# Optimization experiments

Hardware: AMD Instinct MI355X
Metric: run time of the kernel (lower is better)

## Reference

```python
import jax, jax.numpy as jnp
import numpy as np

B, D_IN, D_HID, D_OUT = 32768, 512, 4096, 512
EPS = 1e-12  # F.normalize eps


def setup_inputs() -> dict:
    key = jax.random.key(0)
    ks = jax.random.split(key, 9)
    # Weights scaled up from the original 0.001 init so the norm_max clamp
    # branch is actually exercised (norms vary around the threshold).
    return {
        "x": jax.random.normal(ks[0], (B, D_IN), jnp.float32),
        "in_mean": jax.random.normal(ks[1], (D_IN,), jnp.float32) * 0.1,
        "in_std": jax.random.uniform(ks[2], (D_IN,), jnp.float32, 0.5, 1.5),
        "out_mean": jax.random.normal(ks[3], (D_OUT,), jnp.float32) * 0.1,
        "out_std": jax.random.uniform(ks[4], (D_OUT,), jnp.float32, 0.5, 1.5),
        "W1": jax.random.normal(ks[5], (D_HID, D_IN), jnp.float32) * 0.02,
        "b1": jax.random.normal(ks[6], (D_HID,), jnp.float32) * 0.001,
        "W2": jax.random.normal(ks[7], (D_OUT, D_HID), jnp.float32) * 0.02,
        "b2": jax.random.normal(ks[8], (D_OUT,), jnp.float32) * 0.001,
        "norm_max": 1,
    }


def reference(x, in_mean, in_std, out_mean, out_std, W1, b1, W2, b2, norm_max):
    norm_max = jnp.float32(norm_max)
    x_copy = x[..., :512]
    # input normalization
    xn = (x - in_mean) / in_std
    # 2-layer MLP: Linear -> ReLU -> Linear
    h = jax.nn.relu(jnp.einsum("bi,hi->bh", xn, W1) + b1)
    res = jnp.einsum("bh,oh->bo", h, W2) + b2
    # vectorized per-row norm clamp (torch loop: rescale rows with norm > norm_max)
    norms = jnp.linalg.norm(res, axis=-1, keepdims=True)  # [B,1]
    scale = norm_max / jax.lax.stop_gradient(norms)
    res = jnp.where(norms > norm_max, res * scale, res)
    # output de-normalization (torch subtracts norm_input[0] here)
    res = res * out_std + out_mean - in_mean
    # residual + L2 normalize
    mapped = res + x_copy
    mnorm = jnp.linalg.norm(mapped, axis=-1, keepdims=True)
    return mapped / jnp.maximum(mnorm, EPS)
```

## Files before the change

### kernel.cpp

```cpp
#include <hip/hip_runtime.h>
#include <hip/hip_bf16.h>

#define NB 32768
#define DIN 512
#define DHID 4096
#define DOUT 512

typedef __attribute__((ext_vector_type(8))) __bf16 bf16x8;
typedef __attribute__((ext_vector_type(4))) float f32x4;

__device__ __forceinline__ unsigned short f2bf(float f) {
  unsigned u = __builtin_bit_cast(unsigned, f);
  u += 0x7FFFu + ((u >> 16) & 1u);
  return (unsigned short)(u >> 16);
}

__device__ __forceinline__ void gload16(void* lds, const void* g) {
  __builtin_amdgcn_global_load_lds(
      (const __attribute__((address_space(1))) void*)g,
      (__attribute__((address_space(3))) void*)lds, 16, 0, 0);
}

__global__ __launch_bounds__(256) void k_prep_x(
    const float4* __restrict__ x, const float* __restrict__ mean,
    const float* __restrict__ stdv, ushort4* __restrict__ xn) {
  const int i = blockIdx.x * 256 + threadIdx.x;
  const int col = (i << 2) & (DIN - 1);
  const float4 v = x[i];
  const float4 m = *(const float4*)(mean + col);
  const float4 s = *(const float4*)(stdv + col);
  ushort4 o;
  o.x = f2bf((v.x - m.x) / s.x);
  o.y = f2bf((v.y - m.y) / s.y);
  o.z = f2bf((v.z - m.z) / s.z);
  o.w = f2bf((v.w - m.w) / s.w);
  xn[i] = o;
}

__global__ __launch_bounds__(256) void k_cvt(
    const float4* __restrict__ in, ushort4* __restrict__ out) {
  const int i = blockIdx.x * 256 + threadIdx.x;
  const float4 v = in[i];
  ushort4 o;
  o.x = f2bf(v.x); o.y = f2bf(v.y); o.z = f2bf(v.z); o.w = f2bf(v.w);
  out[i] = o;
}

__global__ __launch_bounds__(512, 2) void k_gemm1(
    const unsigned short* __restrict__ A, const unsigned short* __restrict__ W,
    const float* __restrict__ bias, unsigned short* __restrict__ outp,
    const int N, const int K, const int nbn) {
  __shared__ __align__(16) char lds[3 * 49152];
  const int tid = threadIdx.x;
  const int wave = tid >> 6, lane = tid & 63;
  const int wm = wave >> 1, wn = wave & 1;
  const int lidlo = lane & 15, lidhi = lane >> 4;

  const int nwg = (int)gridDim.x;
  const int wg = (int)blockIdx.x;
  const int q = nwg >> 3, r = nwg & 7;
  const int xcd = wg & 7, loc = wg >> 3;
  const int swz = (xcd < r ? xcd * (q + 1) : r * (q + 1) + (xcd - r) * q) + loc;
  const int bm = swz / nbn, bn = swz % nbn;
  const int R0 = bm * 256, C0 = bn * 128;

  const int NT = K >> 6;
  const int dbase0 = wave * 1024;

  auto STAGE = [&](int t, int s) {
    char* as = lds + s * 49152;
    char* bs = as + 32768;
    const int k0 = t << 6;
#pragma unroll
    for (int i = 0; i < 4; ++i) {
      const int db = i * 8192 + dbase0;
      const int d = db + lane * 16;
      const int row = d >> 7;
      const int colb = (d & 127) ^ ((row & 7) << 4);
      gload16(as + db,
              (const char*)A + ((size_t)(R0 + row) * K + k0) * 2 + colb);
    }
#pragma unroll
    for (int i = 0; i < 2; ++i) {
      const int db = i * 8192 + dbase0;
      const int d = db + lane * 16;
      const int row = d >> 7;
      const int colb = (d & 127) ^ ((row & 7) << 4);
      gload16(bs + db,
              (const char*)W + ((size_t)(C0 + row) * K + k0) * 2 + colb);
    }
  };

  f32x4 acc[4][4] = {};

  STAGE(0, 0);
  STAGE(1, 1);
  asm volatile("s_waitcnt vmcnt(6)" ::: "memory");
  __builtin_amdgcn_s_barrier();

  int slot = 0;
  for (int t = 0; t < NT; ++t) {
    const int nslot = (slot == 2) ? 0 : slot + 1;
    const int sslot = (nslot == 2) ? 0 : nslot + 1;
    if (t + 2 < NT) STAGE(t + 2, sslot);

    const char* as = lds + slot * 49152;
    const char* bs = as + 32768;
    bf16x8 af[2][4], bw[2][4];
#pragma unroll
    for (int kk = 0; kk < 2; ++kk) {
#pragma unroll
      for (int i = 0; i < 4; ++i) {
        const int ra = wm * 64 + i * 16 + lidlo;
        af[kk][i] = *(const bf16x8*)(
            as + ra * 128 + ((kk * 64 + lidhi * 16) ^ ((ra & 7) << 4)));
        const int rb = wn * 64 + i * 16 + lidlo;
        bw[kk][i] = *(const bf16x8*)(
            bs + rb * 128 + ((kk * 64 + lidhi * 16) ^ ((rb & 7) << 4)));
      }
    }
    __builtin_amdgcn_s_setprio(1);
#pragma unroll
    for (int kk = 0; kk < 2; ++kk)
#pragma unroll
      for (int i = 0; i < 4; ++i)
#pragma unroll
        for (int j = 0; j < 4; ++j)
          acc[i][j] = __builtin_amdgcn_mfma_f32_16x16x32_bf16(
              af[kk][i], bw[kk][j], acc[i][j], 0, 0, 0);
    __builtin_amdgcn_s_setprio(0);

    if (t + 2 < NT) {
      asm volatile("s_waitcnt vmcnt(6)" ::: "memory");
    } else {
      asm volatile("s_waitcnt vmcnt(0)" ::: "memory");
    }
    __builtin_amdgcn_s_barrier();
    slot = nslot;
  }

  const int m0 = R0 + wm * 64 + (lidhi << 2);
  const int n0 = C0 + wn * 64 + lidlo;
#pragma unroll
  for (int j = 0; j < 4; ++j) {
    const int n = n0 + j * 16;
    const float bv = bias[n];
#pragma unroll
    for (int i = 0; i < 4; ++i) {
#pragma unroll
      for (int rr = 0; rr < 4; ++rr) {
        const int m = m0 + i * 16 + rr;
        float v = fmaxf(acc[i][j][rr] + bv, 0.0f);
        outp[(size_t)m * N + n] = f2bf(v);
      }
    }
  }
}

__global__ __launch_bounds__(512, 2) void k_gemm2(
    const unsigned short* __restrict__ A, const unsigned short* __restrict__ W,
    const float* __restrict__ bias, float* __restrict__ outp, const int K) {
  __shared__ __align__(16) char lds[2 * 81920];
  const int tid = threadIdx.x;
  const int wave = tid >> 6, lane = tid & 63;
  const int wm = wave >> 2, wn = wave & 3;
  const int lidlo = lane & 15, lidhi = lane >> 4;

  const int nwg = (int)gridDim.x;
  const int wg = (int)blockIdx.x;
  const int q = nwg >> 3, r = nwg & 7;
  const int xcd = wg & 7, loc = wg >> 3;
  const int bm = (xcd < r ? xcd * (q + 1) : r * (q + 1) + (xcd - r) * q) + loc;
  const int R0 = bm * 128;

  const int NT = K >> 6;

  auto STAGE = [&](int t, int s) {
    char* as = lds + s * 81920;
    char* bs = as + 16384;
    const int k0 = t << 6;
#pragma unroll
    for (int i = 0; i < 10; ++i) {
      const int c = wave * 10 + i;
      if (c < 16) {
        const int d = c * 1024 + lane * 16;
        const int row = d >> 7;
        const int colb = (d & 127) ^ ((row & 7) << 4);
        gload16(as + c * 1024,
                (const char*)A + ((size_t)(R0 + row) * K + k0) * 2 + colb);
      } else {
        const int d = (c - 16) * 1024 + lane * 16;
        const int row = d >> 7;
        const int colb = (d & 127) ^ ((row & 7) << 4);
        gload16(bs + (c - 16) * 1024,
                (const char*)W + ((size_t)row * K + k0) * 2 + colb);
      }
    }
  };

  f32x4 acc[4][8] = {};

  STAGE(0, 0);
  asm volatile("s_waitcnt vmcnt(0)" ::: "memory");
  __builtin_amdgcn_s_barrier();

  for (int t = 0; t < NT; ++t) {
    if (t + 1 < NT) STAGE(t + 1, (t + 1) & 1);
    const char* as = lds + (t & 1) * 81920;
    const char* bs = as + 16384;
#pragma unroll
    for (int kk = 0; kk < 2; ++kk) {
      bf16x8 af[4], bw[8];
#pragma unroll
      for (int i = 0; i < 4; ++i) {
        const int ra = wm * 64 + i * 16 + lidlo;
        af[i] = *(const bf16x8*)(
            as + ra * 128 + ((kk * 64 + lidhi * 16) ^ ((ra & 7) << 4)));
      }
#pragma unroll
      for (int j = 0; j < 8; ++j) {
        const int rb = wn * 128 + j * 16 + lidlo;
        bw[j] = *(const bf16x8*)(
            bs + rb * 128 + ((kk * 64 + lidhi * 16) ^ ((rb & 7) << 4)));
      }
      __builtin_amdgcn_s_setprio(1);
#pragma unroll
      for (int i = 0; i < 4; ++i)
#pragma unroll
        for (int j = 0; j < 8; ++j)
          acc[i][j] = __builtin_amdgcn_mfma_f32_16x16x32_bf16(
              af[i], bw[j], acc[i][j], 0, 0, 0);
      __builtin_amdgcn_s_setprio(0);
    }
    asm volatile("s_waitcnt vmcnt(0)" ::: "memory");
    __builtin_amdgcn_s_barrier();
  }

  const int m0 = R0 + wm * 64 + (lidhi << 2);
  const int n0 = wn * 128 + lidlo;
#pragma unroll
  for (int j = 0; j < 8; ++j) {
    const int n = n0 + j * 16;
    const float bv = bias[n];
#pragma unroll
    for (int i = 0; i < 4; ++i) {
#pragma unroll
      for (int rr = 0; rr < 4; ++rr) {
        const int m = m0 + i * 16 + rr;
        outp[(size_t)m * DOUT + n] = acc[i][j][rr] + bv;
      }
    }
  }
}

__global__ __launch_bounds__(256) void k_finalize(
    float* __restrict__ res, const float* __restrict__ x,
    const float* __restrict__ out_mean, const float* __restrict__ out_std,
    const float* __restrict__ in_mean, const int* __restrict__ nmp) {
  const int wave = threadIdx.x >> 6, lane = threadIdx.x & 63;
  const size_t row = (size_t)blockIdx.x * 4 + wave;
  const float nm = (float)(*nmp);
  const size_t base = row * DOUT + (size_t)lane * 8;
  const int c = lane * 8;
  const float4 r0 = *(const float4*)(res + base);
  const float4 r1 = *(const float4*)(res + base + 4);
  float ss = r0.x * r0.x + r0.y * r0.y + r0.z * r0.z + r0.w * r0.w +
             r1.x * r1.x + r1.y * r1.y + r1.z * r1.z + r1.w * r1.w;
#pragma unroll
  for (int o = 32; o > 0; o >>= 1) ss += __shfl_xor(ss, o);
  const float rn = sqrtf(ss);
  const float sc = (rn > nm) ? (nm / rn) : 1.0f;
  const float4 os0 = *(const float4*)(out_std + c);
  const float4 os1 = *(const float4*)(out_std + c + 4);
  const float4 om0 = *(const float4*)(out_mean + c);
  const float4 om1 = *(const float4*)(out_mean + c + 4);
  const float4 im0 = *(const float4*)(in_mean + c);
  const float4 im1 = *(const float4*)(in_mean + c + 4);
  const float4 x0 = *(const float4*)(x + base);
  const float4 x1 = *(const float4*)(x + base + 4);
  float4 m0, m1;
  m0.x = r0.x * sc * os0.x + om0.x - im0.x + x0.x;
  m0.y = r0.y * sc * os0.y + om0.y - im0.y + x0.y;
  m0.z = r0.z * sc * os0.z + om0.z - im0.z + x0.z;
  m0.w = r0.w * sc * os0.w + om0.w - im0.w + x0.w;
  m1.x = r1.x * sc * os1.x + om1.x - im1.x + x1.x;
  m1.y = r1.y * sc * os1.y + om1.y - im1.y + x1.y;
  m1.z = r1.z * sc * os1.z + om1.z - im1.z + x1.z;
  m1.w = r1.w * sc * os1.w + om1.w - im1.w + x1.w;
  float s2 = m0.x * m0.x + m0.y * m0.y + m0.z * m0.z + m0.w * m0.w +
             m1.x * m1.x + m1.y * m1.y + m1.z * m1.z + m1.w * m1.w;
#pragma unroll
  for (int o = 32; o > 0; o >>= 1) s2 += __shfl_xor(s2, o);
  const float inv = 1.0f / fmaxf(sqrtf(s2), 1e-12f);
  float4 o0, o1;
  o0.x = m0.x * inv; o0.y = m0.y * inv; o0.z = m0.z * inv; o0.w = m0.w * inv;
  o1.x = m1.x * inv; o1.y = m1.y * inv; o1.z = m1.z * inv; o1.w = m1.w * inv;
  *(float4*)(res + base) = o0;
  *(float4*)(res + base + 4) = o1;
}

extern "C" void kernel_launch(void* const* d_in, const int* in_sizes, int n_in,
                              void* d_out, int out_size, void* d_ws, size_t ws_size,
                              hipStream_t stream) {
  const float* x = (const float*)d_in[0];
  const float* in_mean = (const float*)d_in[1];
  const float* in_std = (const float*)d_in[2];
  const float* out_mean = (const float*)d_in[3];
  const float* out_std = (const float*)d_in[4];
  const float* W1 = (const float*)d_in[5];
  const float* b1 = (const float*)d_in[6];
  const float* W2 = (const float*)d_in[7];
  const float* b2 = (const float*)d_in[8];
  const int* nmp = (const int*)d_in[9];
  float* out = (float*)d_out;

  char* ws = (char*)d_ws;
  unsigned short* xn = (unsigned short*)ws;   ws += (size_t)NB * DIN * 2;
  unsigned short* W1b = (unsigned short*)ws;  ws += (size_t)DHID * DIN * 2;
  unsigned short* W2b = (unsigned short*)ws;  ws += (size_t)DOUT * DHID * 2;
  unsigned short* h = (unsigned short*)ws;

  const size_t fixedB = (size_t)(ws - (char*)d_ws);
  const size_t avail = (ws_size > fixedB) ? (ws_size - fixedB) : 0;
  long long crows = (long long)(avail / ((size_t)DHID * 2));
  if (crows > NB) crows = NB;
  crows &= ~255LL;
  if (crows < 256) crows = 256;
  const int chunk = (int)crows;

  k_prep_x<<<16384, 256, 0, stream>>>((const float4*)x, in_mean, in_std,
                                      (ushort4*)xn);
  k_cvt<<<2048, 256, 0, stream>>>((const float4*)W1, (ushort4*)W1b);
  k_cvt<<<2048, 256, 0, stream>>>((const float4*)W2, (ushort4*)W2b);

  for (int s = 0; s < NB; s += chunk) {
    const int mc = (NB - s < chunk) ? (NB - s) : chunk;
    const int g1 = (mc / 256) * (DHID / 128);
    k_gemm1<<<g1, 512, 0, stream>>>(xn + (size_t)s * DIN, W1b, b1, h,
                                    DHID, DIN, DHID / 128);
    const int g2 = mc / 128;
    k_gemm2<<<g2, 512, 0, stream>>>(h, W2b, b2, out + (size_t)s * DOUT, DHID);
  }

  k_finalize<<<NB / 4, 256, 0, stream>>>(out, x, out_mean, out_std, in_mean, nmp);
}
```

Measured before the change: 509.0 us.

## Fuse norm clamp, denormalization, residual and L2 normalize into gemm2 epilogue

Moves the finalize kernel's per-row norm clamp, output de-normalization, residual add and L2 normalization into the epilogue of the second GEMM. Row norms are reduced with lane shuffles and then combined across the four column waves through LDS. This removes a separate launch and a full fp32 write and reread of the GEMM output. In exchange the epilogue gains extra barriers, register pressure and less-coalesced strided loads of x.

```diff
diff --git a/kernel.cpp b/kernel.cpp
--- a/kernel.cpp
+++ b/kernel.cpp
@@ -159,7 +159,10 @@
 
 __global__ __launch_bounds__(512, 2) void k_gemm2(
     const unsigned short* __restrict__ A, const unsigned short* __restrict__ W,
-    const float* __restrict__ bias, float* __restrict__ outp, const int K) {
+    const float* __restrict__ bias, const float* __restrict__ x,
+    const float* __restrict__ out_mean, const float* __restrict__ out_std,
+    const float* __restrict__ in_mean, const int* __restrict__ nmp,
+    float* __restrict__ outp, const int K) {
   __shared__ __align__(16) char lds[2 * 81920];
   const int tid = threadIdx.x;
   const int wave = tid >> 6, lane = tid & 63;
@@ -236,67 +239,100 @@
     __builtin_amdgcn_s_barrier();
   }
 
-  const int m0 = R0 + wm * 64 + (lidhi << 2);
+  float* red = (float*)lds;
   const int n0 = wn * 128 + lidlo;
+  float bv[8], os[8], omim[8];
 #pragma unroll
   for (int j = 0; j < 8; ++j) {
     const int n = n0 + j * 16;
-    const float bv = bias[n];
-#pragma unroll
-    for (int i = 0; i < 4; ++i) {
-#pragma unroll
-      for (int rr = 0; rr < 4; ++rr) {
-        const int m = m0 + i * 16 + rr;
-        outp[(size_t)m * DOUT + n] = acc[i][j][rr] + bv;
-      }
-    }
-  }
-}
-
-__global__ __launch_bounds__(256) void k_finalize(
-    float* __restrict__ res, const float* __restrict__ x,
-    const float* __restrict__ out_mean, const float* __restrict__ out_std,
-    const float* __restrict__ in_mean, const int* __restrict__ nmp) {
-  const int wave = threadIdx.x >> 6, lane = threadIdx.x & 63;
-  const size_t row = (size_t)blockIdx.x * 4 + wave;
+    bv[j] = bias[n];
+    os[j] = out_std[n];
+    omim[j] = out_mean[n] - in_mean[n];
+  }
   const float nm = (float)(*nmp);
-  const size_t base = row * DOUT + (size_t)lane * 8;
-  const int c = lane * 8;
-  const float4 r0 = *(const float4*)(res + base);
-  const float4 r1 = *(const float4*)(res + base + 4);
-  float ss = r0.x * r0.x + r0.y * r0.y + r0.z * r0.z + r0.w * r0.w +
-             r1.x * r1.x + r1.y * r1.y + r1.z * r1.z + r1.w * r1.w;
-#pragma unroll
-  for (int o = 32; o > 0; o >>= 1) ss += __shfl_xor(ss, o);
-  const float rn = sqrtf(ss);
-  const float sc = (rn > nm) ? (nm / rn) : 1.0f;
-  const float4 os0 = *(const float4*)(out_std + c);
-  const float4 os1 = *(const float4*)(out_std + c + 4);
-  const float4 om0 = *(const float4*)(out_mean + c);
-  const float4 om1 = *(const float4*)(out_mean + c + 4);
-  const float4 im0 = *(const float4*)(in_mean + c);
-  const float4 im1 = *(const float4*)(in_mean + c + 4);
-  const float4 x0 = *(const float4*)(x + base);
-  const float4 x1 = *(const float4*)(x + base + 4);
-  float4 m0, m1;
-  m0.x = r0.x * sc * os0.x + om0.x - im0.x + x0.x;
-  m0.y = r0.y * sc * os0.y + om0.y - im0.y + x0.y;
-  m0.z = r0.z * sc * os0.z + om0.z - im0.z + x0.z;
-  m0.w = r0.w * sc * os0.w + om0.w - im0.w + x0.w;
-  m1.x = r1.x * sc * os1.x + om1.x - im1.x + x1.x;
-  m1.y = r1.y * sc * os1.y + om1.y - im1.y + x1.y;
-  m1.z = r1.z * sc * os1.z + om1.z - im1.z + x1.z;
-  m1.w = r1.w * sc * os1.w + om1.w - im1.w + x1.w;
-  float s2 = m0.x * m0.x + m0.y * m0.y + m0.z * m0.z + m0.w * m0.w +
-             m1.x * m1.x + m1.y * m1.y + m1.z * m1.z + m1.w * m1.w;
-#pragma unroll
-  for (int o = 32; o > 0; o >>= 1) s2 += __shfl_xor(s2, o);
-  const float inv = 1.0f / fmaxf(sqrtf(s2), 1e-12f);
-  float4 o0, o1;
-  o0.x = m0.x * inv; o0.y = m0.y * inv; o0.z = m0.z * inv; o0.w = m0.w * inv;
-  o1.x = m1.x * inv; o1.y = m1.y * inv; o1.z = m1.z * inv; o1.w = m1.w * inv;
-  *(float4*)(res + base) = o0;
-  *(float4*)(res + base + 4) = o1;
+  const int lmb = wm * 64 + (lidhi << 2);
+
+  float scr[4][4];
+#pragma unroll
+  for (int i = 0; i < 4; ++i) {
+#pragma unroll
+    for (int rr = 0; rr < 4; ++rr) {
+      float s = 0.0f;
+#pragma unroll
+      for (int j = 0; j < 8; ++j) {
+        const float v = acc[i][j][rr] + bv[j];
+        acc[i][j][rr] = v;
+        s += v * v;
+      }
+      s += __shfl_xor(s, 1); s += __shfl_xor(s, 2);
+      s += __shfl_xor(s, 4); s += __shfl_xor(s, 8);
+      scr[i][rr] = s;
+    }
+  }
+  if (lidlo == 0) {
+#pragma unroll
+    for (int i = 0; i < 4; ++i)
+#pragma unroll
+      for (int rr = 0; rr < 4; ++rr)
+        red[wn * 128 + lmb + i * 16 + rr] = scr[i][rr];
+  }
+  __syncthreads();
+#pragma unroll
+  for (int i = 0; i < 4; ++i) {
+#pragma unroll
+    for (int rr = 0; rr < 4; ++rr) {
+      const int lm = lmb + i * 16 + rr;
+      const float t = red[lm] + red[128 + lm] + red[256 + lm] + red[384 + lm];
+      const float rn = sqrtf(t);
+      scr[i][rr] = (rn > nm) ? (nm / rn) : 1.0f;
+    }
+  }
+  __syncthreads();
+
+  float s2a[4][4];
+#pragma unroll
+  for (int i = 0; i < 4; ++i) {
+#pragma unroll
+    for (int rr = 0; rr < 4; ++rr) {
+      const int row = R0 + lmb + i * 16 + rr;
+      const float sc = scr[i][rr];
+      float s = 0.0f;
+#pragma unroll
+      for (int j = 0; j < 8; ++j) {
+        const int n = n0 + j * 16;
+        const float mv = acc[i][j][rr] * sc * os[j] + omim[j] +
+                         x[(size_t)row * DOUT + n];
+        acc[i][j][rr] = mv;
+        s += mv * mv;
+      }
+      s += __shfl_xor(s, 1); s += __shfl_xor(s, 2);
+      s += __shfl_xor(s, 4); s += __shfl_xor(s, 8);
+      s2a[i][rr] = s;
+    }
+  }
+  if (lidlo == 0) {
+#pragma unroll
+    for (int i = 0; i < 4; ++i)
+#pragma unroll
+      for (int rr = 0; rr < 4; ++rr)
+        red[wn * 128 + lmb + i * 16 + rr] = s2a[i][rr];
+  }
+  __syncthreads();
+#pragma unroll
+  for (int i = 0; i < 4; ++i) {
+#pragma unroll
+    for (int rr = 0; rr < 4; ++rr) {
+      const int lm = lmb + i * 16 + rr;
+      const float t = red[lm] + red[128 + lm] + red[256 + lm] + red[384 + lm];
+      const float inv = 1.0f / fmaxf(sqrtf(t), 1e-12f);
+      const int row = R0 + lm;
+#pragma unroll
+      for (int j = 0; j < 8; ++j) {
+        const int n = n0 + j * 16;
+        outp[(size_t)row * DOUT + n] = acc[i][j][rr] * inv;
+      }
+    }
+  }
 }
 
 extern "C" void kernel_launch(void* const* d_in, const int* in_sizes, int n_in,
@@ -339,8 +375,8 @@
     k_gemm1<<<g1, 512, 0, stream>>>(xn + (size_t)s * DIN, W1b, b1, h,
                                     DHID, DIN, DHID / 128);
     const int g2 = mc / 128;
-    k_gemm2<<<g2, 512, 0, stream>>>(h, W2b, b2, out + (size_t)s * DOUT, DHID);
-  }
-
-  k_finalize<<<NB / 4, 256, 0, stream>>>(out, x, out_mean, out_std, in_mean, nmp);
-}
+    k_gemm2<<<g2, 512, 0, stream>>>(h, W2b, b2, x + (size_t)s * DIN,
+                                    out_mean, out_std, in_mean, nmp,
+                                    out + (size_t)s * DOUT, DHID);
+  }
+}
```

Result: faster. 474.0 us (-6.9%).
